# Performance work log

Measured on AMD Instinct MI355X. Metric: run time of the kernel, lower is better.

The kernel has to match this reference:

```python
import jax, jax.numpy as jnp
from jax import lax
import numpy as np

B = 512          # batch
M = 2000         # num_memories
CC = 16          # conv_channel_size
F = CC * 4 * 6 * 6  # 2304 feature size
BN_EPS = 1e-5
COS_EPS = 1e-8
SHRINK_EPS = 0.01


def conv(x, w, b, stride, pad):
    y = lax.conv_general_dilated(x, w, (stride, stride), [(pad, pad), (pad, pad)],
                                 dimension_numbers=('NCHW', 'OIHW', 'NCHW'))
    return y + b[None, :, None, None]


def deconv(x, w, b, stride, pad, out_pad):
    # w is torch ConvTranspose2d layout: (in, out, kh, kw)
    k = w.shape[2]
    w2 = jnp.flip(w, (2, 3)).transpose(1, 0, 2, 3)  # (out, in, kh, kw)
    p = [(k - 1 - pad, k - 1 - pad + out_pad)] * 2
    y = lax.conv_general_dilated(x, w2, (1, 1), p, lhs_dilation=(stride, stride),
                                 dimension_numbers=('NCHW', 'OIHW', 'NCHW'))
    return y + b[None, :, None, None]


def bn(x, g, b):
    # BatchNorm2d in training mode: per-channel batch statistics (biased var)
    m = x.mean((0, 2, 3), keepdims=True)
    v = x.var((0, 2, 3), keepdims=True)
    return g[None, :, None, None] * (x - m) * lax.rsqrt(v + BN_EPS) + b[None, :, None, None]


def setup_inputs() -> dict:
    key = jax.random.key(0)
    ks = jax.random.split(key, 16)
    rn = lambda k, s, sc=0.05: jax.random.normal(k, s, jnp.float32) * sc
    return {
        'x': jax.random.uniform(ks[0], (B, 1, 96, 96), jnp.float32),
        'c1_w': rn(ks[1], (16, 1, 1, 1), 0.3), 'c1_b': jnp.zeros(16),
        'bn1_g': jnp.ones(16), 'bn1_b': jnp.zeros(16),
        'c2_w': rn(ks[2], (32, 16, 3, 3)), 'c2_b': jnp.zeros(32),
        'bn2_g': jnp.ones(32), 'bn2_b': jnp.zeros(32),
        'c3_w': rn(ks[3], (64, 32, 3, 3)), 'c3_b': jnp.zeros(64),
        'bn3_g': jnp.ones(64), 'bn3_b': jnp.zeros(64),
        'c4_w': rn(ks[4], (64, 64, 3, 3)), 'c4_b': jnp.zeros(64),
        'bn4_g': jnp.ones(64), 'bn4_b': jnp.zeros(64),
        'memory': rn(ks[5], (M, F), 0.03),
        'd0_w': rn(ks[6], (64, 64, 3, 3)), 'd0_b': jnp.zeros(64),
        'dbn0_g': jnp.ones(64), 'dbn0_b': jnp.zeros(64),
        'd1_w': rn(ks[7], (64, 32, 3, 3)), 'd1_b': jnp.zeros(32),
        'dbn1_g': jnp.ones(32), 'dbn1_b': jnp.zeros(32),
        'd2_w': rn(ks[8], (32, 16, 2, 2)), 'd2_b': jnp.zeros(16),
        'dbn2_g': jnp.ones(16), 'dbn2_b': jnp.zeros(16),
        'd3_w': rn(ks[9], (16, 1, 2, 2)), 'd3_b': jnp.zeros(1),
    }


def reference(x, c1_w, c1_b, bn1_g, bn1_b, c2_w, c2_b, bn2_g, bn2_b,
              c3_w, c3_b, bn3_g, bn3_b, c4_w, c4_b, bn4_g, bn4_b, memory,
              d0_w, d0_b, dbn0_g, dbn0_b, d1_w, d1_b, dbn1_g, dbn1_b,
              d2_w, d2_b, dbn2_g, dbn2_b, d3_w, d3_b):
    relu = jax.nn.relu
    # Encoder: 96 -> 49 -> 25 -> 13 -> 6
    h = relu(bn(conv(x, c1_w, c1_b, 2, 1), bn1_g, bn1_b))
    h = relu(bn(conv(h, c2_w, c2_b, 2, 1), bn2_g, bn2_b))
    h = relu(bn(conv(h, c3_w, c3_b, 2, 1), bn3_g, bn3_b))
    h = relu(bn(conv(h, c4_w, c4_b, 2, 0), bn4_g, bn4_b))
    z = h.reshape(h.shape[0], -1)  # (B, 2304)

    # Memory addressing: cosine similarity without materializing (B, M, F)
    zn = jnp.linalg.norm(z, axis=1)          # (B,)
    mn = jnp.linalg.norm(memory, axis=1)     # (M,)
    sim = (z @ memory.T) / jnp.maximum(zn[:, None] * mn[None, :], COS_EPS)
    w = jax.nn.softmax(sim, axis=1)
    # Sparse hard-shrink addressing + L1 renorm
    t = 1.0 / memory.shape[0]
    w = relu(w - t) * w / (jnp.abs(w - t) + SHRINK_EPS)
    w = w / jnp.sum(jnp.abs(w), axis=1, keepdims=True)
    z_hat = w @ memory  # (B, F)

    # Decoder: 6 -> 13 -> 25 -> 49 -> 98
    g = z_hat.reshape(-1, 64, 6, 6)
    g = relu(bn(deconv(g, d0_w, d0_b, 2, 0, 0), dbn0_g, dbn0_b))
    g = relu(bn(deconv(g, d1_w, d1_b, 2, 1, 0), dbn1_g, dbn1_b))
    g = relu(bn(deconv(g, d2_w, d2_b, 2, 1, 1), dbn2_g, dbn2_b))
    g = jax.nn.sigmoid(deconv(g, d3_w, d3_b, 2, 0, 0))
    return g
```

## Files before the change

kernel.cpp:

```cpp
#include <hip/hip_runtime.h>
#include <stdint.h>


typedef unsigned short ushort_t;
typedef __bf16 bf16x8 __attribute__((ext_vector_type(8)));
typedef float f32x4 __attribute__((ext_vector_type(4)));

#define DEV static __device__ __forceinline__

DEV ushort_t f2bf(float f){
  union { float f; uint32_t u; } v; v.f = f;
  return (ushort_t)((v.u + 0x7FFFu + ((v.u >> 16) & 1u)) >> 16);
}
DEV float bf2f(ushort_t u){
  union { uint32_t u; float f; } v; v.u = ((uint32_t)u) << 16;
  return v.f;
}

DEV uint32_t affine2(uint32_t rw, const float* ac, int ci, int nch){
  float lo = bf2f((ushort_t)(rw & 0xffffu));
  float hi = bf2f((ushort_t)(rw >> 16));
  lo = fmaxf(fmaf(ac[ci],   lo, ac[nch+ci]),   0.f);
  hi = fmaxf(fmaf(ac[ci+1], hi, ac[nch+ci+1]), 0.f);
  return (uint32_t)f2bf(lo) | ((uint32_t)f2bf(hi) << 16);
}
DEV uint4 stage_chunk(uint4 raw, const float* ac, int ci0, int nch){
  uint4 o;
  o.x = affine2(raw.x, ac, ci0+0, nch);
  o.y = affine2(raw.y, ac, ci0+2, nch);
  o.z = affine2(raw.z, ac, ci0+4, nch);
  o.w = affine2(raw.w, ac, ci0+6, nch);
  return o;
}

#define H_XS   0
#define H_S2   64
#define H_Q2   96
#define H_S3   192
#define H_Q3   256
#define H_S4   448
#define H_Q4   512
#define H_DS0  704
#define H_DQ0  768
#define H_DS1  960
#define H_DQ1  992
#define H_DS2  1088
#define H_DQ2  1104
#define H_ZN   1152
#define H_MN   1664
#define H_BUK  4096
#define NBUK   16
#define BSTRIDE 1280
#define HDR_FLOATS (H_BUK + NBUK*BSTRIDE)

#define OW2 0
#define OW3 5120
#define OW4 23552
#define OD0 60416
#define OD1 97280
#define OD2 115712
#define NWPK 117760

#define SIMSTRIDE 1024000
#define ZHSTRIDE  1179648
#define NSPL 4

#define PREP_XS 256
#define PREP_W2 (PREP_XS + 460)
#define PREP_TOT (PREP_W2 + 63*18)

DEV float* bkt(float* hdr, int blk){ return hdr + H_BUK + (size_t)(blk & (NBUK-1))*BSTRIDE; }

DEV void coef_lds(const float* __restrict__ hdr, int offS, int offQ,
                  const float* __restrict__ g, const float* __restrict__ be,
                  float* ac, int nch, float invN, int tid){
  if (tid < nch){
    float s = 0.f, q = 0.f;
    #pragma unroll
    for (int k=0;k<NBUK;k++){
      s += hdr[H_BUK + k*BSTRIDE + offS + tid];
      q += hdr[H_BUK + k*BSTRIDE + offQ + tid];
    }
    float m = s*invN;
    float v = q*invN - m*m;
    float a = g[tid]*rsqrtf(v + 1e-5f);
    ac[tid] = a;
    ac[nch+tid] = be[tid] - m*a;
  }
}

__global__ __launch_bounds__(256) void k_prep(
    const float* __restrict__ mem, ushort_t* __restrict__ mbf, ushort_t* __restrict__ mt,
    float* __restrict__ hdr,
    const float* __restrict__ c2w, const float* __restrict__ c3w, const float* __restrict__ c4w,
    const float* __restrict__ d0w, const float* __restrict__ d1w, const float* __restrict__ d2w,
    ushort_t* __restrict__ WPK, const float* __restrict__ x){
  __shared__ ushort_t smu[32*132];
  const int blk = blockIdx.x, tid = threadIdx.x;
  if (blk < PREP_XS){
    float* sm = (float*)smu;
    float s = 0.f, q = 0.f;
    const int total = 512*49*49;
    for (int idx = blk*256 + tid; idx < total; idx += 256*256){
      int b = idx / 2401;
      int r = idx - b*2401;
      int i = r / 49, j = r - i*49;
      float v = 0.f;
      if (i > 0 && j > 0) v = x[(size_t)b*9216 + (2*i-1)*96 + (2*j-1)];
      s += v; q += v*v;
    }
    for (int o=32;o;o>>=1){ s += __shfl_down(s,o,64); q += __shfl_down(q,o,64); }
    int w = tid>>6;
    if ((tid&63)==0){ sm[w*2]=s; sm[w*2+1]=q; }
    __syncthreads();
    if (tid==0){
      float* bk = bkt(hdr, blk);
      atomicAdd(&bk[H_XS+0], sm[0]+sm[2]+sm[4]+sm[6]);
      atomicAdd(&bk[H_XS+1], sm[1]+sm[3]+sm[5]+sm[7]);
    }
  } else if (blk < PREP_W2){
    int i = (blk - PREP_XS)*256 + tid;
    if (i >= NWPK) return;
    float val = 0.f;
    if (i < OW3){
      int co = i/160, k = i - co*160, tap = k>>4, ci = k&15;
      if (tap < 9) val = c2w[(co*16+ci)*9+tap];
    } else if (i < OW4){
      int r = i - OW3; int co = r/288, k = r - co*288, tap = k>>5, ci = k&31;
      val = c3w[(co*32+ci)*9+tap];
    } else if (i < OD0){
      int r = i - OW4; int co = r/576, k = r - co*576, tap = k>>6, ci = k&63;
      val = c4w[(co*64+ci)*9+tap];
    } else if (i < OD1){
      int r = i - OD0;
      const int base[4]={0,16384,24576,32768}, K[4]={256,128,128,64};
      const int T0[4][4] = {{0,2,6,8},{1,7,0,0},{3,5,0,0},{4,0,0,0}};
      int cl = (r<16384)?0:(r<24576)?1:(r<32768)?2:3;
      int rr = r - base[cl]; int co = rr/K[cl], k = rr - co*K[cl], t = k>>6, ci = k&63;
      val = d0w[(ci*64+co)*9 + T0[cl][t]];
    } else if (i < OD2){
      int r = i - OD1;
      const int base[4]={0,2048,6144,10240}, K[4]={64,128,128,256};
      const int T1[4][4] = {{4,0,0,0},{3,5,0,0},{1,7,0,0},{0,2,6,8}};
      int cl = (r<2048)?0:(r<6144)?1:(r<10240)?2:3;
      int rr = r - base[cl]; int co = rr/K[cl], k = rr - co*K[cl], t = k>>6, ci = k&63;
      val = d1w[(ci*32+co)*9 + T1[cl][t]];
    } else {
      int r = i - OD2;
      int cl = r>>9, s = r&511, co = s>>5, ci = s&31;
      const int pis[4]={0,0,1,1}, pjs[4]={0,1,0,1};
      val = d2w[((ci*16+co)*2 + (1-pis[cl]))*2 + (1-pjs[cl])];
    }
    WPK[i] = f2bf(val);
  } else {
    const int mb = blk - PREP_W2;
    const int ft = mb % 18, mtile = mb / 18;
    const int tx = tid & 31, ty = tid >> 5;
    #pragma unroll
    for (int r0=0;r0<4;r0++){
      int m = mtile*32 + r0*8 + ty;
      int f = ft*128 + tx*4;
      f32x4 v = {0.f,0.f,0.f,0.f};
      if (m < 2000) v = *(const f32x4*)&mem[(size_t)m*2304 + f];
      ushort_t h0=f2bf(v[0]), h1=f2bf(v[1]), h2=f2bf(v[2]), h3=f2bf(v[3]);
      uint2 pk = make_uint2((uint32_t)h0 | ((uint32_t)h1<<16), (uint32_t)h2 | ((uint32_t)h3<<16));
      *(uint2*)&smu[(r0*8+ty)*132 + tx*4] = pk;
      if (m < 2000) *(uint2*)&mbf[(size_t)m*2304 + f] = pk;
      float p = v[0]*v[0] + v[1]*v[1] + v[2]*v[2] + v[3]*v[3];
      for (int o=16;o;o>>=1) p += __shfl_down(p, o, 32);
      if (tx==0 && m<2000) atomicAdd(&hdr[H_MN+m], p);
    }
    __syncthreads();
    #pragma unroll
    for (int ff=0; ff<16; ff++){
      int fl = ff*8 + ty;
      mt[(size_t)(ft*128 + fl)*2016 + mtile*32 + tx] = smu[tx*132 + fl];
    }
  }
}

__global__ __launch_bounds__(256) void k_conv2m(
    const float* __restrict__ x, const ushort_t* __restrict__ WPK, const float* __restrict__ b2g,
    const float* __restrict__ c1w, const float* __restrict__ c1b,
    const float* __restrict__ bn1g, const float* __restrict__ bn1b,
    float* __restrict__ hdr, ushort_t* __restrict__ out){
  __shared__ ushort_t inp[27*51*16];
  __shared__ float ac[32];
  const int blk = blockIdx.x, b = blk>>1, h = blk&1, tid = threadIdx.x;
  const int ro = h*13, nr = h?12:13, npos = nr*25, ntiles = (npos+15)>>4;
  if (tid < 16){
    float sx=0.f, qx=0.f;
    #pragma unroll
    for (int k=0;k<NBUK;k++){ sx += hdr[H_BUK+k*BSTRIDE+H_XS]; qx += hdr[H_BUK+k*BSTRIDE+H_XS+1]; }
    const float N = 512.f*49.f*49.f;
    float mx = sx/N, vx = qx/N - mx*mx;
    float mean = c1w[tid]*mx + c1b[tid];
    float a = bn1g[tid]*rsqrtf(c1w[tid]*c1w[tid]*vx + 1e-5f);
    ac[tid] = a*c1w[tid];
    ac[16+tid] = a*(c1b[tid]-mean) + bn1b[tid];
  }
  __syncthreads();
  for (int e = tid; e < 27*51; e += 256){
    int lr = e/51, gc = e - lr*51;
    int grg = 2*ro + lr;
    bool inside = (grg>=1 && grg<=49 && gc>=1 && gc<=49);
    float v = 0.f;
    if (grg>=2 && grg<=49 && gc>=2 && gc<=49) v = x[(size_t)b*9216 + (2*grg-3)*96 + (2*gc-3)];
    ushort_t hv[16];
    if (inside){
      #pragma unroll
      for (int c=0;c<16;c++) hv[c] = f2bf(fmaxf(fmaf(ac[c], v, ac[16+c]), 0.f));
    } else {
      #pragma unroll
      for (int c=0;c<16;c++) hv[c] = 0;
    }
    uint32_t w0[8];
    #pragma unroll
    for (int c=0;c<8;c++) w0[c] = (uint32_t)hv[2*c] | ((uint32_t)hv[2*c+1]<<16);
    uint4* dst = (uint4*)&inp[e*16];
    dst[0] = make_uint4(w0[0],w0[1],w0[2],w0[3]);
    dst[1] = make_uint4(w0[4],w0[5],w0[6],w0[7]);
  }
  __syncthreads();
  const int wv = tid>>6, lane = tid&63, r = lane&15, q = lane>>4;
  const int cotile = wv&1;
  bf16x8 af[5];
  #pragma unroll
  for (int c=0;c<5;c++) af[c] = *(const bf16x8*)(WPK + OW2 + (cotile*16+r)*160 + c*32 + q*8);
  float biasr[4];
  #pragma unroll
  for (int v=0;v<4;v++) biasr[v] = b2g[cotile*16 + q*4 + v];
  const int TOFF[10] = {0,1,2,51,52,53,102,103,104,0};
  const int qhi = q>>1, ci0 = (q&1)*8;
  float sacc[4]={0,0,0,0}, qacc[4]={0,0,0,0};
  for (int t = wv>>1; t < ntiles; t += 2){
    int p = t*16 + r;
    bool ok = p < npos;
    int pc = ok ? p : 0;
    int a_ = pc/25, c_ = pc - a_*25;
    int pb = (2*a_)*51 + 2*c_;
    f32x4 acc = {0.f,0.f,0.f,0.f};
    #pragma unroll
    for (int c=0;c<5;c++){
      int toff = qhi ? TOFF[2*c+1] : TOFF[2*c];
      bf16x8 bv = *(const bf16x8*)&inp[(pb + toff)*16 + ci0];
      acc = __builtin_amdgcn_mfma_f32_16x16x32_bf16(af[c], bv, acc, 0, 0, 0);
    }
    if (ok){
      int pg = (ro + a_)*25 + c_;
      ushort_t pk[4];
      #pragma unroll
      for (int reg=0;reg<4;reg++){
        float y = acc[reg] + biasr[reg];
        pk[reg] = f2bf(y);
        sacc[reg] += y; qacc[reg] += y*y;
      }
      *(uint2*)&out[((size_t)b*625 + pg)*32 + cotile*16 + q*4] =
        make_uint2((uint32_t)pk[0] | ((uint32_t)pk[1]<<16), (uint32_t)pk[2] | ((uint32_t)pk[3]<<16));
    }
  }
  float* bk = bkt(hdr, blk);
  #pragma unroll
  for (int reg=0;reg<4;reg++){
    float s = sacc[reg], qq = qacc[reg];
    for (int o=8;o;o>>=1){ s += __shfl_down(s,o,16); qq += __shfl_down(qq,o,16); }
    if (r==0){ atomicAdd(&bk[H_S2+cotile*16+q*4+reg], s); atomicAdd(&bk[H_Q2+cotile*16+q*4+reg], qq); }
  }
}

__global__ __launch_bounds__(256) void k_conv3m(
    const ushort_t* __restrict__ h2, const ushort_t* __restrict__ WPK, const float* __restrict__ b3g,
    const float* __restrict__ g, const float* __restrict__ be,
    float* __restrict__ hdr, ushort_t* __restrict__ out){
  __shared__ ushort_t inp[15*27*32];
  __shared__ float ac[64];
  const int blk = blockIdx.x, b = blk>>1, h = blk&1, tid = threadIdx.x;
  const int a0 = h*7, na = h?6:7, npos = na*13, ntiles = (npos+15)>>4, nrows = 2*na+1;
  coef_lds(hdr, H_S2, H_Q2, g, be, ac, 32, 1.f/(512.f*625.f), tid);
  __syncthreads();
  for (int e = tid; e < nrows*27*4; e += 256){
    int cell = e>>2, ch = e&3;
    int lr = cell/27, lc = cell - lr*27;
    int ii = 2*a0 - 1 + lr, j = lc - 1;
    uint4 val = make_uint4(0,0,0,0);
    if ((unsigned)ii < 25u && (unsigned)j < 25u){
      uint4 raw = *(const uint4*)&h2[((size_t)b*625 + ii*25 + j)*32 + ch*8];
      val = stage_chunk(raw, ac, ch*8, 32);
    }
    int slot = ch ^ ((cell>>1)&3);
    *(uint4*)&inp[cell*32 + slot*8] = val;
  }
  __syncthreads();
  const int wv = tid>>6, lane = tid&63, r = lane&15, q = lane>>4;
  bf16x8 af[9];
  #pragma unroll
  for (int c=0;c<9;c++) af[c] = *(const bf16x8*)(WPK + OW3 + (wv*16+r)*288 + c*32 + q*8);
  float biasr[4];
  #pragma unroll
  for (int v=0;v<4;v++) biasr[v] = b3g[wv*16 + q*4 + v];
  const int TOFF[9] = {0,1,2,27,28,29,54,55,56};
  float sacc[4]={0,0,0,0}, qacc[4]={0,0,0,0};
  for (int t = 0; t < ntiles; t++){
    int p = t*16 + r;
    bool ok = p < npos;
    int pc = ok ? p : 0;
    int a_ = pc/13, c_ = pc - a_*13;
    int pb = (2*a_)*27 + 2*c_;
    f32x4 acc = {0.f,0.f,0.f,0.f};
    #pragma unroll
    for (int c=0;c<9;c++){
      int cell = pb + TOFF[c];
      int slot = q ^ ((cell>>1)&3);
      bf16x8 bv = *(const bf16x8*)&inp[cell*32 + slot*8];
      acc = __builtin_amdgcn_mfma_f32_16x16x32_bf16(af[c], bv, acc, 0, 0, 0);
    }
    if (ok){
      int pos = (a0 + a_)*13 + c_;
      ushort_t pk[4];
      #pragma unroll
      for (int reg=0;reg<4;reg++){
        float y = acc[reg] + biasr[reg];
        pk[reg] = f2bf(y);
        sacc[reg] += y; qacc[reg] += y*y;
      }
      *(uint2*)&out[((size_t)b*169 + pos)*64 + wv*16 + q*4] =
        make_uint2((uint32_t)pk[0] | ((uint32_t)pk[1]<<16), (uint32_t)pk[2] | ((uint32_t)pk[3]<<16));
    }
  }
  float* bk = bkt(hdr, blk);
  #pragma unroll
  for (int reg=0;reg<4;reg++){
    float s = sacc[reg], qq = qacc[reg];
    for (int o=8;o;o>>=1){ s += __shfl_down(s,o,16); qq += __shfl_down(qq,o,16); }
    if (r==0){ atomicAdd(&bk[H_S3+wv*16+q*4+reg], s); atomicAdd(&bk[H_Q3+wv*16+q*4+reg], qq); }
  }
}

__global__ __launch_bounds__(256) void k_conv4m(
    const ushort_t* __restrict__ h3, const ushort_t* __restrict__ WPK, const float* __restrict__ b4g,
    const float* __restrict__ g, const float* __restrict__ be,
    float* __restrict__ hdr, float* __restrict__ out){
  __shared__ ushort_t inp[169*64];
  __shared__ float ac[128];
  const int b = blockIdx.x, tid = threadIdx.x;
  coef_lds(hdr, H_S3, H_Q3, g, be, ac, 64, 1.f/(512.f*169.f), tid);
  __syncthreads();
  for (int e = tid; e < 169*8; e += 256){
    int cell = e>>3, ch = e&7;
    uint4 raw = *(const uint4*)&h3[((size_t)b*169 + cell)*64 + ch*8];
    uint4 val = stage_chunk(raw, ac, ch*8, 64);
    int slot = ch ^ ((cell>>1)&7);
    *(uint4*)&inp[cell*64 + slot*8] = val;
  }
  __syncthreads();
  const int wv = tid>>6, lane = tid&63, r = lane&15, q = lane>>4;
  bf16x8 af[18];
  #pragma unroll
  for (int c=0;c<18;c++) af[c] = *(const bf16x8*)(WPK + OW4 + (wv*16+r)*576 + c*32 + q*8);
  float biasr[4];
  #pragma unroll
  for (int v=0;v<4;v++) biasr[v] = b4g[wv*16 + q*4 + v];
  const int TOFF[9] = {0,1,2,13,14,15,26,27,28};
  float sacc[4]={0,0,0,0}, qacc[4]={0,0,0,0};
  for (int t = 0; t < 3; t++){
    int p = t*16 + r;
    bool ok = p < 36;
    int pc = ok ? p : 0;
    int a_ = pc/6, c_ = pc - a_*6;
    int pb = (2*a_)*13 + 2*c_;
    f32x4 acc = {0.f,0.f,0.f,0.f};
    #pragma unroll
    for (int c=0;c<18;c++){
      int cell = pb + TOFF[c>>1];
      int chunk = (c&1)*4 + q;
      int slot = chunk ^ ((cell>>1)&7);
      bf16x8 bv = *(const bf16x8*)&inp[cell*64 + slot*8];
      acc = __builtin_amdgcn_mfma_f32_16x16x32_bf16(af[c], bv, acc, 0, 0, 0);
    }
    if (ok){
      #pragma unroll
      for (int reg=0;reg<4;reg++){
        float y = acc[reg] + biasr[reg];
        out[((size_t)b*64 + wv*16 + q*4 + reg)*36 + p] = y;
        sacc[reg] += y; qacc[reg] += y*y;
      }
    }
  }
  float* bk = bkt(hdr, b);
  #pragma unroll
  for (int reg=0;reg<4;reg++){
    float s = sacc[reg], qq = qacc[reg];
    for (int o=8;o;o>>=1){ s += __shfl_down(s,o,16); qq += __shfl_down(qq,o,16); }
    if (r==0){ atomicAdd(&bk[H_S4+wv*16+q*4+reg], s); atomicAdd(&bk[H_Q4+wv*16+q*4+reg], qq); }
  }
}

__global__ __launch_bounds__(256) void k_gemmA(
    const float* __restrict__ ZR, const ushort_t* __restrict__ Bm, float* __restrict__ D,
    const float* __restrict__ g, const float* __restrict__ be, float* __restrict__ hdr){
  __shared__ __align__(16) ushort_t lB[128*40];
  __shared__ __align__(16) ushort_t lA[128*40];
  __shared__ float ac[128];
  const int blk = blockIdx.x;
  const int s = blk >> 6, t = blk & 63;
  const int bi = t >> 4, bj = t & 15;
  const int m0 = bi*128, n0 = bj*128;
  const int k0 = s*18, k1 = k0 + 18;
  const int tid = threadIdx.x;
  coef_lds(hdr, H_S4, H_Q4, g, be, ac, 64, 1.f/(512.f*36.f), tid);
  const int lane = tid & 63, wv = tid >> 6;
  const int r = lane & 15, q = lane >> 4;
  const int wr = wv >> 1, wc = wv & 1;
  const bool bj0 = (bj == 0);
  float* Ds = D + (size_t)s*SIMSTRIDE;
  const int srow = tid >> 1, skq = (tid & 1) * 16;
  const bool bok = (n0 + srow) < 2000;
  const ushort_t* pb = Bm + (size_t)(n0 + srow)*2304 + skq;
  const float*    pa = ZR + (size_t)(m0 + srow)*2304 + skq;
  uint4* wB = (uint4*)&lB[srow*40 + skq];
  uint4* wA = (uint4*)&lA[srow*40 + skq];
  const uint4 zz = make_uint4(0,0,0,0);
  uint4 rb0 = bok ? *(const uint4*)(pb + (size_t)k0*32)     : zz;
  uint4 rb1 = bok ? *(const uint4*)(pb + (size_t)k0*32 + 8) : zz;
  f32x4 raA[4];
  #pragma unroll
  for (int i=0;i<4;i++) raA[i] = *(const f32x4*)(pa + (size_t)k0*32 + i*4);
  f32x4 acc[4][4];
  #pragma unroll
  for (int i=0;i<4;i++)
    #pragma unroll
    for (int j=0;j<4;j++) acc[i][j] = (f32x4){0.f,0.f,0.f,0.f};
  float zsq = 0.f;
  __syncthreads();
  for (int k=k0; k<k1; k++){
    if (k > k0) __syncthreads();
    wB[0] = rb0; wB[1] = rb1;
    {
      const int kb = k*32 + skq;
      uint32_t pw[8];
      #pragma unroll
      for (int jj=0;jj<8;jj++){
        float v0 = raA[jj>>1][(jj&1)*2+0];
        float v1 = raA[jj>>1][(jj&1)*2+1];
        int c0 = (kb + 2*jj) / 36;
        int c1 = (kb + 2*jj + 1) / 36;
        float h0 = fmaxf(fmaf(ac[c0], v0, ac[64+c0]), 0.f);
        float h1 = fmaxf(fmaf(ac[c1], v1, ac[64+c1]), 0.f);
        if (bj0) zsq += h0*h0 + h1*h1;
        pw[jj] = (uint32_t)f2bf(h0) | ((uint32_t)f2bf(h1) << 16);
      }
      wA[0] = make_uint4(pw[0],pw[1],pw[2],pw[3]);
      wA[1] = make_uint4(pw[4],pw[5],pw[6],pw[7]);
    }
    if (k+1 < k1){
      const ushort_t* nb = pb + (size_t)(k+1)*32;
      rb0 = bok ? *(const uint4*)(nb)     : zz;
      rb1 = bok ? *(const uint4*)(nb + 8) : zz;
      const float* na = pa + (size_t)(k+1)*32;
      #pragma unroll
      for (int i=0;i<4;i++) raA[i] = *(const f32x4*)(na + i*4);
    }
    __syncthreads();
    bf16x8 aF[4], bF[4];
    #pragma unroll
    for (int mt=0;mt<4;mt++) aF[mt] = *(const bf16x8*)&lA[(wr*64+mt*16+r)*40 + q*8];
    #pragma unroll
    for (int nt=0;nt<4;nt++) bF[nt] = *(const bf16x8*)&lB[(wc*64+nt*16+r)*40 + q*8];
    #pragma unroll
    for (int mt=0;mt<4;mt++)
      #pragma unroll
      for (int nt=0;nt<4;nt++)
        acc[mt][nt] = __builtin_amdgcn_mfma_f32_16x16x32_bf16(aF[mt], bF[nt], acc[mt][nt], 0, 0, 0);
  }
  if (bj0){
    zsq += __shfl_down(zsq, 1, 64);
    if ((tid & 1) == 0) atomicAdd(&hdr[H_ZN + m0 + srow], zsq);
  }
  #pragma unroll
  for (int mt=0;mt<4;mt++){
    int row = m0 + wr*64 + mt*16 + q*4;
    #pragma unroll
    for (int nt=0;nt<4;nt++){
      int col = n0 + wc*64 + nt*16 + r;
      if (col < 2000){
        #pragma unroll
        for (int reg=0;reg<4;reg++)
          Ds[(size_t)(row+reg)*2000 + col] = acc[mt][nt][reg];
      }
    }
  }
}

__global__ __launch_bounds__(256) void k_gemmB(const ushort_t* __restrict__ A, const ushort_t* __restrict__ Bm,
                                               float* __restrict__ D, int Nb, int N, int Kp, int kch,
                                               int tiles, int ksp, size_t dstride){
  __shared__ __align__(16) ushort_t lB[128*40];
  const int blk = blockIdx.x;
  const int s = blk / tiles, t = blk - s*tiles;
  const int bi = t / Nb, bj = t - bi*Nb;
  const int m0 = bi*128, n0 = bj*128;
  const int k0 = s*ksp, k1 = min(kch, k0 + ksp);
  const int tid = threadIdx.x;
  const int lane = tid & 63, wv = tid >> 6;
  const int r = lane & 15, q = lane >> 4;
  const int wr = wv >> 1, wc = wv & 1;
  float* Ds = D + (size_t)s*dstride;
  const int srow = tid >> 1, skq = (tid & 1) * 16;
  const bool bok = (n0 + srow) < N;
  const ushort_t* pb = Bm + (size_t)(n0 + srow)*Kp + skq;
  uint4* wB = (uint4*)&lB[srow*40 + skq];
  const uint4 zz = make_uint4(0,0,0,0);
  uint4 rb0 = bok ? *(const uint4*)(pb + k0*32)     : zz;
  uint4 rb1 = bok ? *(const uint4*)(pb + k0*32 + 8) : zz;
  const ushort_t* pa = A + (size_t)(m0 + wr*64 + r)*Kp + q*8;
  bf16x8 aN[4];
  #pragma unroll
  for (int mt=0;mt<4;mt++) aN[mt] = *(const bf16x8*)(pa + k0*32 + (size_t)(mt*16)*Kp);
  f32x4 acc[4][4];
  #pragma unroll
  for (int i=0;i<4;i++)
    #pragma unroll
    for (int j=0;j<4;j++) acc[i][j] = (f32x4){0.f,0.f,0.f,0.f};
  for (int k=k0; k<k1; k++){
    if (k > k0) __syncthreads();
    wB[0] = rb0; wB[1] = rb1;
    bf16x8 aF[4];
    #pragma unroll
    for (int mt=0;mt<4;mt++) aF[mt] = aN[mt];
    if (k+1 < k1){
      const ushort_t* nb = pb + (k+1)*32;
      rb0 = bok ? *(const uint4*)(nb)     : zz;
      rb1 = bok ? *(const uint4*)(nb + 8) : zz;
      const ushort_t* na = pa + (k+1)*32;
      #pragma unroll
      for (int mt=0;mt<4;mt++) aN[mt] = *(const bf16x8*)(na + (size_t)(mt*16)*Kp);
    }
    __syncthreads();
    bf16x8 bF[4];
    #pragma unroll
    for (int nt=0;nt<4;nt++) bF[nt] = *(const bf16x8*)&lB[(wc*64+nt*16+r)*40 + q*8];
    #pragma unroll
    for (int mt=0;mt<4;mt++)
      #pragma unroll
      for (int nt=0;nt<4;nt++)
        acc[mt][nt] = __builtin_amdgcn_mfma_f32_16x16x32_bf16(aF[mt], bF[nt], acc[mt][nt], 0, 0, 0);
  }
  #pragma unroll
  for (int mt=0;mt<4;mt++){
    int row = m0 + wr*64 + mt*16 + q*4;
    #pragma unroll
    for (int nt=0;nt<4;nt++){
      int col = n0 + wc*64 + nt*16 + r;
      if (col < N){
        #pragma unroll
        for (int reg=0;reg<4;reg++)
          Ds[(size_t)(row+reg)*N + col] = acc[mt][nt][reg];
      }
    }
  }
}

__global__ __launch_bounds__(256) void k_softmax(const float* __restrict__ sim, float* __restrict__ hdr,
                                                 ushort_t* __restrict__ wbf){
  __shared__ float e[2000];
  __shared__ float red[8];
  const int b = blockIdx.x, tid = threadIdx.x;
  const float znb = sqrtf(hdr[H_ZN+b]);
  float part = 0.f;
  for (int m=tid;m<2000;m+=256){
    size_t ix = (size_t)b*2000+m;
    float sv = 0.f;
    #pragma unroll
    for (int j=0;j<NSPL;j++) sv += sim[ix + (size_t)j*SIMSTRIDE];
    float mnb = sqrtf(hdr[H_MN+m]);
    float s = sv / fmaxf(znb * mnb, 1e-8f);
    float ev = __expf(s);
    e[m] = ev; part += ev;
  }
  for (int o=32;o;o>>=1) part += __shfl_down(part,o,64);
  if ((tid&63)==0) red[tid>>6] = part;
  __syncthreads();
  const float denom = red[0]+red[1]+red[2]+red[3];
  const float t = 1.0f/2000.0f;
  float part2 = 0.f;
  for (int m=tid;m<2000;m+=256){
    float w = e[m]/denom;
    float d = w - t;
    float sh = fmaxf(d,0.f)*w/(fabsf(d)+0.01f);
    e[m] = sh; part2 += sh;
  }
  for (int o=32;o;o>>=1) part2 += __shfl_down(part2,o,64);
  if ((tid&63)==0) red[4+(tid>>6)] = part2;
  __syncthreads();
  const float inv = 1.0f/(red[4]+red[5]+red[6]+red[7]);
  for (int m=tid;m<2016;m+=256){
    ushort_t o = 0;
    if (m < 2000) o = f2bf(e[m]*inv);
    wbf[(size_t)b*2016+m] = o;
  }
}

__global__ __launch_bounds__(256) void k_deconv0m(
    const float* __restrict__ zh, const ushort_t* __restrict__ WPK, const float* __restrict__ b0g,
    float* __restrict__ hdr, ushort_t* __restrict__ out){
  __shared__ ushort_t inp[64*64];
  const int b = blockIdx.x, tid = threadIdx.x;
  for (int i = tid; i < 512; i += 256) ((uint4*)inp)[i] = make_uint4(0,0,0,0);
  __syncthreads();
  for (int i = tid; i < 576; i += 256){
    int idx = i*4;
    f32x4 v = *(const f32x4*)&zh[(size_t)b*2304 + idx];
    #pragma unroll
    for (int j=1;j<NSPL;j++)
      v += *(const f32x4*)&zh[(size_t)b*2304 + idx + (size_t)j*ZHSTRIDE];
    int ci = idx/36;
    int p  = idx - ci*36;
    int chunk = ci >> 3, cil = ci & 7;
    #pragma unroll
    for (int e2=0;e2<4;e2++){
      int pp = p + e2;
      int r6 = pp/6, c6 = pp - r6*6;
      int cell = (r6+1)*8 + (c6+1);
      int slot = chunk ^ ((cell>>1)&7);
      inp[cell*64 + slot*8 + cil] = f2bf(v[e2]);
    }
  }
  __syncthreads();
  const int wv = tid>>6, lane = tid&63, r = lane&15, q = lane>>4;
  float biasr[4];
  #pragma unroll
  for (int v=0;v<4;v++) biasr[v] = b0g[wv*16 + q*4 + v];
  const int NCOL[4]={7,6,7,6}, NPOS[4]={49,42,42,36}, NT[4]={4,3,3,3},
            NCH[4]={8,4,4,2}, KB[4]={0,16384,24576,32768}, KK[4]={256,128,128,64},
            PI[4]={0,0,1,1}, PJ[4]={0,1,0,1};
  const int TOFF[4][4] = {{9,8,1,0},{9,1,0,0},{9,8,0,0},{9,0,0,0}};
  float sacc[4]={0,0,0,0}, qacc[4]={0,0,0,0};
  #pragma unroll
  for (int cl=0; cl<4; cl++){
    bf16x8 af[8];
    #pragma unroll
    for (int m=0;m<NCH[cl];m++)
      af[m] = *(const bf16x8*)(WPK + OD0 + KB[cl] + (wv*16+r)*KK[cl] + m*32 + q*8);
    for (int t = 0; t < NT[cl]; t++){
      int p = t*16 + r;
      bool ok = p < NPOS[cl];
      int pc = ok ? p : 0;
      int a_ = pc/NCOL[cl], c_ = pc - a_*NCOL[cl];
      int pb = a_*8 + c_;
      f32x4 acc = {0.f,0.f,0.f,0.f};
      #pragma unroll
      for (int m=0;m<NCH[cl];m++){
        int cell = pb + TOFF[cl][m>>1];
        int chunk = (m&1)*4 + q;
        int slot = chunk ^ ((cell>>1)&7);
        bf16x8 bv = *(const bf16x8*)&inp[cell*64 + slot*8];
        acc = __builtin_amdgcn_mfma_f32_16x16x32_bf16(af[m], bv, acc, 0, 0, 0);
      }
      if (ok){
        int pos = (2*a_+PI[cl])*13 + (2*c_+PJ[cl]);
        ushort_t pk[4];
        #pragma unroll
        for (int reg=0;reg<4;reg++){
          float y = acc[reg] + biasr[reg];
          pk[reg] = f2bf(y);
          sacc[reg] += y; qacc[reg] += y*y;
        }
        *(uint2*)&out[((size_t)b*169 + pos)*64 + wv*16 + q*4] =
          make_uint2((uint32_t)pk[0] | ((uint32_t)pk[1]<<16), (uint32_t)pk[2] | ((uint32_t)pk[3]<<16));
      }
    }
  }
  float* bk = bkt(hdr, b);
  #pragma unroll
  for (int reg=0;reg<4;reg++){
    float s = sacc[reg], qq = qacc[reg];
    for (int o=8;o;o>>=1){ s += __shfl_down(s,o,16); qq += __shfl_down(qq,o,16); }
    if (r==0){ atomicAdd(&bk[H_DS0+wv*16+q*4+reg], s); atomicAdd(&bk[H_DQ0+wv*16+q*4+reg], qq); }
  }
}

__global__ __launch_bounds__(256) void k_deconv1m(
    const ushort_t* __restrict__ g0, const ushort_t* __restrict__ WPK, const float* __restrict__ b1g,
    const float* __restrict__ g, const float* __restrict__ be,
    float* __restrict__ hdr, ushort_t* __restrict__ out){
  __shared__ ushort_t inp[169*64];
  __shared__ float ac[128];
  const int b = blockIdx.x, tid = threadIdx.x;
  coef_lds(hdr, H_DS0, H_DQ0, g, be, ac, 64, 1.f/(512.f*169.f), tid);
  __syncthreads();
  for (int e = tid; e < 169*8; e += 256){
    int cell = e>>3, ch = e&7;
    uint4 raw = *(const uint4*)&g0[((size_t)b*169 + cell)*64 + ch*8];
    uint4 val = stage_chunk(raw, ac, ch*8, 64);
    int slot = ch ^ ((cell>>1)&7);
    *(uint4*)&inp[cell*64 + slot*8] = val;
  }
  __syncthreads();
  const int wv = tid>>6, lane = tid&63, r = lane&15, q = lane>>4;
  const int cotile = wv&1, ph = wv>>1;
  float biasr[4];
  #pragma unroll
  for (int v=0;v<4;v++) biasr[v] = b1g[cotile*16 + q*4 + v];
  const int NCOL[4]={13,12,13,12}, NPOS[4]={169,156,156,144}, NT[4]={11,10,10,9},
            NCH[4]={2,4,4,8}, KB[4]={0,2048,6144,10240}, KK[4]={64,128,128,256},
            PI[4]={0,0,1,1}, PJ[4]={0,1,0,1};
  const int TOFF[4][4] = {{0,0,0,0},{1,0,0,0},{13,0,0,0},{14,13,1,0}};
  float sacc[4]={0,0,0,0}, qacc[4]={0,0,0,0};
  #pragma unroll
  for (int cl=0; cl<4; cl++){
    bf16x8 af[8];
    #pragma unroll
    for (int m=0;m<NCH[cl];m++)
      af[m] = *(const bf16x8*)(WPK + OD1 + KB[cl] + (cotile*16+r)*KK[cl] + m*32 + q*8);
    for (int t = ph; t < NT[cl]; t += 2){
      int p = t*16 + r;
      bool ok = p < NPOS[cl];
      int pc = ok ? p : 0;
      int a_ = pc/NCOL[cl], c_ = pc - a_*NCOL[cl];
      int pb = a_*13 + c_;
      f32x4 acc = {0.f,0.f,0.f,0.f};
      #pragma unroll
      for (int m=0;m<NCH[cl];m++){
        int cell = pb + TOFF[cl][m>>1];
        int chunk = (m&1)*4 + q;
        int slot = chunk ^ ((cell>>1)&7);
        bf16x8 bv = *(const bf16x8*)&inp[cell*64 + slot*8];
        acc = __builtin_amdgcn_mfma_f32_16x16x32_bf16(af[m], bv, acc, 0, 0, 0);
      }
      if (ok){
        int pos = (2*a_+PI[cl])*25 + (2*c_+PJ[cl]);
        ushort_t pk[4];
        #pragma unroll
        for (int reg=0;reg<4;reg++){
          float y = acc[reg] + biasr[reg];
          pk[reg] = f2bf(y);
          sacc[reg] += y; qacc[reg] += y*y;
        }
        *(uint2*)&out[((size_t)b*625 + pos)*32 + cotile*16 + q*4] =
          make_uint2((uint32_t)pk[0] | ((uint32_t)pk[1]<<16), (uint32_t)pk[2] | ((uint32_t)pk[3]<<16));
      }
    }
  }
  float* bk = bkt(hdr, b);
  #pragma unroll
  for (int reg=0;reg<4;reg++){
    float s = sacc[reg], qq = qacc[reg];
    for (int o=8;o;o>>=1){ s += __shfl_down(s,o,16); qq += __shfl_down(qq,o,16); }
    if (r==0){ atomicAdd(&bk[H_DS1+cotile*16+q*4+reg], s); atomicAdd(&bk[H_DQ1+cotile*16+q*4+reg], qq); }
  }
}

__global__ __launch_bounds__(256) void k_deconv2m(
    const ushort_t* __restrict__ g1, const ushort_t* __restrict__ WPK, const float* __restrict__ bg,
    const float* __restrict__ g, const float* __restrict__ be,
    float* __restrict__ hdr, ushort_t* __restrict__ out){
  __shared__ ushort_t inp[625*32];
  __shared__ float ac[64];
  const int b = blockIdx.x, tid = threadIdx.x;
  coef_lds(hdr, H_DS1, H_DQ1, g, be, ac, 32, 1.f/(512.f*625.f), tid);
  __syncthreads();
  for (int e = tid; e < 625*4; e += 256){
    int cell = e>>2, ch = e&3;
    uint4 raw = *(const uint4*)&g1[((size_t)b*625 + cell)*32 + ch*8];
    uint4 val = stage_chunk(raw, ac, ch*8, 32);
    int slot = ch ^ ((cell>>1)&3);
    *(uint4*)&inp[cell*32 + slot*8] = val;
  }
  __syncthreads();
  const int wv = tid>>6, lane = tid&63, r = lane&15, q = lane>>4;
  const int cl = wv;
  float biasr[4];
  #pragma unroll
  for (int v=0;v<4;v++) biasr[v] = bg[q*4 + v];
  const int NCOL[4]={25,24,25,24}, NPOS[4]={625,600,600,576}, NT[4]={40,38,38,36},
            TOFF[4]={0,1,25,26};
  const int nc = NCOL[cl], npos = NPOS[cl], nt = NT[cl], toff = TOFF[cl];
  bf16x8 af = *(const bf16x8*)(WPK + OD2 + cl*512 + r*32 + q*8);
  float sacc[4]={0,0,0,0}, qacc[4]={0,0,0,0};
  for (int t = 0; t < nt; t++){
    int p = t*16 + r;
    bool ok = p < npos;
    int pc = ok ? p : 0;
    int a_ = pc/nc, c_ = pc - a_*nc;
    int cell = a_*25 + c_ + toff;
    int slot = q ^ ((cell>>1)&3);
    f32x4 acc = {0.f,0.f,0.f,0.f};
    bf16x8 bv = *(const bf16x8*)&inp[cell*32 + slot*8];
    acc = __builtin_amdgcn_mfma_f32_16x16x32_bf16(af, bv, acc, 0, 0, 0);
    if (ok){
      ushort_t pk[4];
      #pragma unroll
      for (int reg=0;reg<4;reg++){
        float y = acc[reg] + biasr[reg];
        pk[reg] = f2bf(y);
        sacc[reg] += y; qacc[reg] += y*y;
      }
      *(uint2*)&out[(((size_t)b*4 + cl)*625 + p)*16 + q*4] =
        make_uint2((uint32_t)pk[0] | ((uint32_t)pk[1]<<16), (uint32_t)pk[2] | ((uint32_t)pk[3]<<16));
    }
  }
  float* bk = bkt(hdr, b);
  #pragma unroll
  for (int reg=0;reg<4;reg++){
    float s = sacc[reg], qq = qacc[reg];
    for (int o=8;o;o>>=1){ s += __shfl_down(s,o,16); qq += __shfl_down(qq,o,16); }
    if (r==0){ atomicAdd(&bk[H_DS2+q*4+reg], s); atomicAdd(&bk[H_DQ2+q*4+reg], qq); }
  }
}

__global__ __launch_bounds__(256) void k_deconv3(const ushort_t* __restrict__ g2, const float* __restrict__ w,
                                                 const float* __restrict__ bias,
                                                 const float* __restrict__ g, const float* __restrict__ be,
                                                 float* __restrict__ hdr, float* __restrict__ out){
  __shared__ float ac[32];
  __shared__ float wl[64];
  const int tid = threadIdx.x;
  coef_lds(hdr, H_DS2, H_DQ2, g, be, ac, 16, 1.f/(512.f*2401.f), tid);
  if (tid >= 64 && tid < 128) wl[tid-64] = w[tid-64];
  __syncthreads();
  int idx = blockIdx.x*256 + tid;
  if (idx >= 512*2401) return;
  int b = idx / 2401; int loc = idx - b*2401;
  int ii = loc / 49, jj = loc - ii*49;
  int pi = ii & 1, pj = jj & 1, cl = pi*2 + pj;
  int a = ii >> 1, c = jj >> 1;
  int nc = pj ? 24 : 25;
  const float b0 = bias[0];
  float acc00 = b0, acc01 = b0, acc10 = b0, acc11 = b0;
  const ushort_t* gp = g2 + (((size_t)b*4 + cl)*625 + a*nc + c)*16;
  ushort_t rv[16];
  *(uint4*)&rv[0] = *(const uint4*)(gp);
  *(uint4*)&rv[8] = *(const uint4*)(gp + 8);
  #pragma unroll
  for (int ci=0; ci<16; ci++){
    float raw = bf2f(rv[ci]);
    float h = fmaxf(fmaf(ac[ci], raw, ac[16+ci]), 0.f);
    acc00 = fmaf(h, wl[ci*4+0], acc00);
    acc01 = fmaf(h, wl[ci*4+1], acc01);
    acc10 = fmaf(h, wl[ci*4+2], acc10);
    acc11 = fmaf(h, wl[ci*4+3], acc11);
  }
  float* op = out + (size_t)b*9604 + (2*ii)*98 + 2*jj;
  op[0]   = 1.f/(1.f + __expf(-acc00));
  op[1]   = 1.f/(1.f + __expf(-acc01));
  op[98]  = 1.f/(1.f + __expf(-acc10));
  op[99]  = 1.f/(1.f + __expf(-acc11));
}

extern "C" void kernel_launch(void* const* d_in, const int* in_sizes, int n_in,
                              void* d_out, int out_size, void* d_ws, size_t ws_size,
                              hipStream_t stream){
  (void)in_sizes; (void)n_in; (void)out_size; (void)ws_size;
  const float* x     = (const float*)d_in[0];
  const float* c1w   = (const float*)d_in[1];
  const float* c1b   = (const float*)d_in[2];
  const float* bn1g  = (const float*)d_in[3];
  const float* bn1b  = (const float*)d_in[4];
  const float* c2w   = (const float*)d_in[5];
  const float* c2b   = (const float*)d_in[6];
  const float* bn2g  = (const float*)d_in[7];
  const float* bn2b  = (const float*)d_in[8];
  const float* c3w   = (const float*)d_in[9];
  const float* c3b   = (const float*)d_in[10];
  const float* bn3g  = (const float*)d_in[11];
  const float* bn3b  = (const float*)d_in[12];
  const float* c4w   = (const float*)d_in[13];
  const float* c4b   = (const float*)d_in[14];
  const float* bn4g  = (const float*)d_in[15];
  const float* bn4b  = (const float*)d_in[16];
  const float* mem   = (const float*)d_in[17];
  const float* d0w   = (const float*)d_in[18];
  const float* d0b   = (const float*)d_in[19];
  const float* dbn0g = (const float*)d_in[20];
  const float* dbn0b = (const float*)d_in[21];
  const float* d1w   = (const float*)d_in[22];
  const float* d1b   = (const float*)d_in[23];
  const float* dbn1g = (const float*)d_in[24];
  const float* dbn1b = (const float*)d_in[25];
  const float* d2w   = (const float*)d_in[26];
  const float* d2b   = (const float*)d_in[27];
  const float* dbn2g = (const float*)d_in[28];
  const float* dbn2b = (const float*)d_in[29];
  const float* d3w   = (const float*)d_in[30];
  const float* d3b   = (const float*)d_in[31];

  float* hdr  = (float*)d_ws;
  float* H2f  = hdr + HDR_FLOATS;
  float* H3f  = H2f + 10240000;
  float* ZRAW = H3f + 5537792;
  float* WSLOT= ZRAW + 1179648;
  float* G2   = WSLOT + 73728;
  ushort_t* MEMBF = (ushort_t*)(G2 + 19668992);
  ushort_t* MEMT  = MEMBF + 4608000;
  ushort_t* ZBF   = MEMT + 4644864;
  ushort_t* WBF   = ZBF + 1179648;
  ushort_t* WPK   = (ushort_t*)WSLOT;
  float* SIMP = G2;
  float* ZHP  = G2 + NSPL*SIMSTRIDE;
  ushort_t* G2BF = (ushort_t*)G2;
  ushort_t* H2CL = (ushort_t*)H2f;
  ushort_t* H3CL = (ushort_t*)H3f;
  ushort_t* G0CL = (ushort_t*)H3f;
  ushort_t* G1CL = (ushort_t*)H2f;
  float* OUT = (float*)d_out;

  hipMemsetAsync(hdr, 0, HDR_FLOATS*sizeof(float), stream);
  k_prep     <<<PREP_TOT, 256, 0, stream>>>(mem, MEMBF, MEMT, hdr,
                                            c2w, c3w, c4w, d0w, d1w, d2w, WPK, x);
  k_conv2m   <<<1024, 256, 0, stream>>>(x, WPK, c2b, c1w, c1b, bn1g, bn1b, hdr, H2CL);
  k_conv3m   <<<1024, 256, 0, stream>>>(H2CL, WPK, c3b, bn2g, bn2b, hdr, H3CL);
  k_conv4m   <<<512, 256, 0, stream>>>(H3CL, WPK, c4b, bn3g, bn3b, hdr, ZRAW);
  k_gemmA    <<<256, 256, 0, stream>>>(ZRAW, MEMBF, SIMP, bn4g, bn4b, hdr);
  k_softmax  <<<512, 256, 0, stream>>>(SIMP, hdr, WBF);
  k_gemmB    <<<288, 256, 0, stream>>>(WBF, MEMT, ZHP, 18, 2304, 2016, 63, 72, 16, ZHSTRIDE);
  k_deconv0m <<<512, 256, 0, stream>>>(ZHP, WPK, d0b, hdr, G0CL);
  k_deconv1m <<<512, 256, 0, stream>>>(G0CL, WPK, d1b, dbn0g, dbn0b, hdr, G1CL);
  k_deconv2m <<<512, 256, 0, stream>>>(G1CL, WPK, d2b, dbn1g, dbn1b, hdr, G2BF);
  k_deconv3  <<<4802, 256, 0, stream>>>(G2BF, d3w, d3b, dbn2g, dbn2b, hdr, OUT);
}
```

Measured before the change: 321.5 us.

## Split prep kernel and overlap memory repack with conv2 blocks

The former prep kernel is split. A small first kernel now computes only the input statistics and packs the conv2 weights. The remaining weight packing and the memory bf16 conversion and transpose become extra blocks of the conv2 kernel, so that independent prep work runs alongside conv2 compute instead of before it. This removes the serial prep stage from the critical path. In exchange, conv2 gets heterogeneous blocks, and the repack blocks inherit conv2's large shared-memory allocation, which may limit occupancy.

```diff
diff --git a/kernel.cpp b/kernel.cpp
--- a/kernel.cpp
+++ b/kernel.cpp
@@ -65,9 +65,12 @@
 #define ZHSTRIDE  1179648
 #define NSPL 4
 
-#define PREP_XS 256
-#define PREP_W2 (PREP_XS + 460)
-#define PREP_TOT (PREP_W2 + 63*18)
+#define P0_XS 256
+#define P0_TOT (P0_XS + 20)
+
+#define C2_CONV 1024
+#define C2_WREP (C2_CONV + 440)
+#define C2_TOT  (C2_WREP + 63*18)
 
 DEV float* bkt(float* hdr, int blk){ return hdr + H_BUK + (size_t)(blk & (NBUK-1))*BSTRIDE; }
 
@@ -89,16 +92,12 @@
   }
 }
 
-__global__ __launch_bounds__(256) void k_prep(
-    const float* __restrict__ mem, ushort_t* __restrict__ mbf, ushort_t* __restrict__ mt,
-    float* __restrict__ hdr,
-    const float* __restrict__ c2w, const float* __restrict__ c3w, const float* __restrict__ c4w,
-    const float* __restrict__ d0w, const float* __restrict__ d1w, const float* __restrict__ d2w,
-    ushort_t* __restrict__ WPK, const float* __restrict__ x){
-  __shared__ ushort_t smu[32*132];
+__global__ __launch_bounds__(256) void k_prep0(
+    const float* __restrict__ x, const float* __restrict__ c2w,
+    ushort_t* __restrict__ WPK, float* __restrict__ hdr){
+  __shared__ float sm[8];
   const int blk = blockIdx.x, tid = threadIdx.x;
-  if (blk < PREP_XS){
-    float* sm = (float*)smu;
+  if (blk < P0_XS){
     float s = 0.f, q = 0.f;
     const int total = 512*49*49;
     for (int idx = blk*256 + tid; idx < total; idx += 256*256){
@@ -118,14 +117,56 @@
       atomicAdd(&bk[H_XS+0], sm[0]+sm[2]+sm[4]+sm[6]);
       atomicAdd(&bk[H_XS+1], sm[1]+sm[3]+sm[5]+sm[7]);
     }
-  } else if (blk < PREP_W2){
-    int i = (blk - PREP_XS)*256 + tid;
-    if (i >= NWPK) return;
+  } else {
+    int i = (blk - P0_XS)*256 + tid;
+    int co = i/160, k = i - co*160, tap = k>>4, ci = k&15;
+    float val = (tap < 9) ? c2w[(co*16+ci)*9+tap] : 0.f;
+    WPK[i] = f2bf(val);
+  }
+}
+
+__global__ __launch_bounds__(256) void k_conv2m(
+    const float* __restrict__ x, ushort_t* __restrict__ WPK, const float* __restrict__ b2g,
+    const float* __restrict__ c1w, const float* __restrict__ c1b,
+    const float* __restrict__ bn1g, const float* __restrict__ bn1b,
+    float* __restrict__ hdr, ushort_t* __restrict__ out,
+    const float* __restrict__ c3w, const float* __restrict__ c4w,
+    const float* __restrict__ d0w, const float* __restrict__ d1w, const float* __restrict__ d2w,
+    const float* __restrict__ mem, ushort_t* __restrict__ mbf, ushort_t* __restrict__ mt){
+  __shared__ ushort_t inp[27*51*16];
+  __shared__ float ac[32];
+  const int blk = blockIdx.x, tid = threadIdx.x;
+  if (blk >= C2_WREP){
+    ushort_t* smu = inp;
+    const int mb = blk - C2_WREP;
+    const int ft = mb % 18, mtile = mb / 18;
+    const int tx = tid & 31, ty = tid >> 5;
+    #pragma unroll
+    for (int r0=0;r0<4;r0++){
+      int m = mtile*32 + r0*8 + ty;
+      int f = ft*128 + tx*4;
+      f32x4 v = {0.f,0.f,0.f,0.f};
+      if (m < 2000) v = *(const f32x4*)&mem[(size_t)m*2304 + f];
+      ushort_t h0=f2bf(v[0]), h1=f2bf(v[1]), h2=f2bf(v[2]), h3=f2bf(v[3]);
+      uint2 pk = make_uint2((uint32_t)h0 | ((uint32_t)h1<<16), (uint32_t)h2 | ((uint32_t)h3<<16));
+      *(uint2*)&smu[(r0*8+ty)*132 + tx*4] = pk;
+      if (m < 2000) *(uint2*)&mbf[(size_t)m*2304 + f] = pk;
+      float p = v[0]*v[0] + v[1]*v[1] + v[2]*v[2] + v[3]*v[3];
+      for (int o=16;o;o>>=1) p += __shfl_down(p, o, 32);
+      if (tx==0 && m<2000) atomicAdd(&hdr[H_MN+m], p);
+    }
+    __syncthreads();
+    #pragma unroll
+    for (int ff=0; ff<16; ff++){
+      int fl = ff*8 + ty;
+      mt[(size_t)(ft*128 + fl)*2016 + mtile*32 + tx] = smu[tx*132 + fl];
+    }
+    return;
+  }
+  if (blk >= C2_CONV){
+    int i = OW3 + (blk - C2_CONV)*256 + tid;
     float val = 0.f;
-    if (i < OW3){
-      int co = i/160, k = i - co*160, tap = k>>4, ci = k&15;
-      if (tap < 9) val = c2w[(co*16+ci)*9+tap];
-    } else if (i < OW4){
+    if (i < OW4){
       int r = i - OW3; int co = r/288, k = r - co*288, tap = k>>5, ci = k&31;
       val = c3w[(co*32+ci)*9+tap];
     } else if (i < OD0){
@@ -145,48 +186,16 @@
       int cl = (r<2048)?0:(r<6144)?1:(r<10240)?2:3;
       int rr = r - base[cl]; int co = rr/K[cl], k = rr - co*K[cl], t = k>>6, ci = k&63;
       val = d1w[(ci*32+co)*9 + T1[cl][t]];
-    } else {
+    } else if (i < NWPK){
       int r = i - OD2;
       int cl = r>>9, s = r&511, co = s>>5, ci = s&31;
       const int pis[4]={0,0,1,1}, pjs[4]={0,1,0,1};
       val = d2w[((ci*16+co)*2 + (1-pis[cl]))*2 + (1-pjs[cl])];
     }
-    WPK[i] = f2bf(val);
-  } else {
-    const int mb = blk - PREP_W2;
-    const int ft = mb % 18, mtile = mb / 18;
-    const int tx = tid & 31, ty = tid >> 5;
-    #pragma unroll
-    for (int r0=0;r0<4;r0++){
-      int m = mtile*32 + r0*8 + ty;
-      int f = ft*128 + tx*4;
-      f32x4 v = {0.f,0.f,0.f,0.f};
-      if (m < 2000) v = *(const f32x4*)&mem[(size_t)m*2304 + f];
-      ushort_t h0=f2bf(v[0]), h1=f2bf(v[1]), h2=f2bf(v[2]), h3=f2bf(v[3]);
-      uint2 pk = make_uint2((uint32_t)h0 | ((uint32_t)h1<<16), (uint32_t)h2 | ((uint32_t)h3<<16));
-      *(uint2*)&smu[(r0*8+ty)*132 + tx*4] = pk;
-      if (m < 2000) *(uint2*)&mbf[(size_t)m*2304 + f] = pk;
-      float p = v[0]*v[0] + v[1]*v[1] + v[2]*v[2] + v[3]*v[3];
-      for (int o=16;o;o>>=1) p += __shfl_down(p, o, 32);
-      if (tx==0 && m<2000) atomicAdd(&hdr[H_MN+m], p);
-    }
-    __syncthreads();
-    #pragma unroll
-    for (int ff=0; ff<16; ff++){
-      int fl = ff*8 + ty;
-      mt[(size_t)(ft*128 + fl)*2016 + mtile*32 + tx] = smu[tx*132 + fl];
-    }
-  }
-}
-
-__global__ __launch_bounds__(256) void k_conv2m(
-    const float* __restrict__ x, const ushort_t* __restrict__ WPK, const float* __restrict__ b2g,
-    const float* __restrict__ c1w, const float* __restrict__ c1b,
-    const float* __restrict__ bn1g, const float* __restrict__ bn1b,
-    float* __restrict__ hdr, ushort_t* __restrict__ out){
-  __shared__ ushort_t inp[27*51*16];
-  __shared__ float ac[32];
-  const int blk = blockIdx.x, b = blk>>1, h = blk&1, tid = threadIdx.x;
+    if (i < NWPK) WPK[i] = f2bf(val);
+    return;
+  }
+  const int b = blk>>1, h = blk&1;
   const int ro = h*13, nr = h?12:13, npos = nr*25, ntiles = (npos+15)>>4;
   if (tid < 16){
     float sx=0.f, qx=0.f;
@@ -905,9 +914,9 @@
   float* OUT = (float*)d_out;
 
   hipMemsetAsync(hdr, 0, HDR_FLOATS*sizeof(float), stream);
-  k_prep     <<<PREP_TOT, 256, 0, stream>>>(mem, MEMBF, MEMT, hdr,
-                                            c2w, c3w, c4w, d0w, d1w, d2w, WPK, x);
-  k_conv2m   <<<1024, 256, 0, stream>>>(x, WPK, c2b, c1w, c1b, bn1g, bn1b, hdr, H2CL);
+  k_prep0    <<<P0_TOT, 256, 0, stream>>>(x, c2w, WPK, hdr);
+  k_conv2m   <<<C2_TOT, 256, 0, stream>>>(x, WPK, c2b, c1w, c1b, bn1g, bn1b, hdr, H2CL,
+                                          c3w, c4w, d0w, d1w, d2w, mem, MEMBF, MEMT);
   k_conv3m   <<<1024, 256, 0, stream>>>(H2CL, WPK, c3b, bn2g, bn2b, hdr, H3CL);
   k_conv4m   <<<512, 256, 0, stream>>>(H3CL, WPK, c4b, bn3g, bn3b, hdr, ZRAW);
   k_gemmA    <<<256, 256, 0, stream>>>(ZRAW, MEMBF, SIMP, bn4g, bn4b, hdr);
```

Result: no change. 325.0 us (+1.1%).
